# Kernel tuning notes

Measured on AMD Instinct MI355X. Metric: run time of the kernel, lower is better.

Reference implementation:

```python
import jax, jax.numpy as jnp
import numpy as np

TEMPERATURE = 2.0

def setup_inputs() -> dict:
    key = jax.random.key(0)
    x = jax.random.normal(key, (8192, 512), dtype=jnp.float32)
    return {"x": x}

def reference(x) -> jnp.ndarray:
    # torch.pdist(x, p=2).pow(2) == squared euclidean distance over pairs i<j
    n = x.shape[0]
    sq = jnp.sum(x * x, axis=1)                       # [N]
    d2 = sq[:, None] + sq[None, :] - 2.0 * (x @ x.T)  # [N, N]
    d2 = jnp.maximum(d2, 0.0)                         # numerical clamp
    mask = jnp.triu(jnp.ones((n, n), dtype=jnp.bool_), k=1)  # strict upper tri = pdist pairs
    num_pairs = n * (n - 1) // 2
    e = jnp.where(mask, jnp.exp(-TEMPERATURE * d2), 0.0)
    return jnp.log(jnp.sum(e) / num_pairs)
```

## Files before the change

### kernel.cpp

```cpp
#include <hip/hip_runtime.h>
#include <hip/hip_fp8.h>
#include <math.h>

#define N 8192
#define D 512
#define TT 64
#define NT 2080
#define NEG_INF_SENT (-3.0e38f)
#define SCALE1 0x7F7F7F7F

typedef __attribute__((ext_vector_type(8))) int int8x;
typedef __attribute__((ext_vector_type(16))) float f32x16;

#define AS1 __attribute__((address_space(1)))
#define AS3 __attribute__((address_space(3)))

__device__ inline void lse_merge(float& m1, float& s1, float m2, float s2) {
    float M = fmaxf(m1, m2);
    s1 = s1 * __expf(m1 - M) + s2 * __expf(m2 - M);
    m1 = M;
}

__global__ __launch_bounds__(256) void cast_rowsq_kernel(const float* __restrict__ x,
                                                         unsigned char* __restrict__ xb,
                                                         float* __restrict__ sq) {
#pragma unroll
    for (int g4 = 0; g4 < 4; ++g4) {
        int row = blockIdx.x * 16 + g4 * 4 + (threadIdx.x >> 6);
        int lane = threadIdx.x & 63;
        const float4* xr = (const float4*)(x + (size_t)row * D);
        float4 a = xr[lane * 2], b = xr[lane * 2 + 1];
        float v[8] = {a.x, a.y, a.z, a.w, b.x, b.y, b.z, b.w};
        float s = 0.f;
        unsigned int byt[8];
#pragma unroll
        for (int e = 0; e < 8; ++e) {
            s += v[e] * v[e];
            __hip_fp8_e4m3 f8(v[e]);
            byt[e] = (unsigned int)f8.__x;
        }
        uint2 pk;
        pk.x = byt[0] | (byt[1] << 8) | (byt[2] << 16) | (byt[3] << 24);
        pk.y = byt[4] | (byt[5] << 8) | (byt[6] << 16) | (byt[7] << 24);
        int g = row >> 5, rl = row & 31;
        int c = lane >> 3;
        int l5 = (lane >> 2) & 1;
        int h = (lane >> 1) & 1;
        int bb = (lane & 1) << 3;
        size_t addr = ((size_t)((g * 8 + c) * 2 + h) << 10) + ((l5 * 32 + rl) << 4) + bb;
        *(uint2*)(xb + addr) = pk;
#pragma unroll
        for (int off = 32; off > 0; off >>= 1) s += __shfl_down(s, off, 64);
        if (lane == 0) sq[row] = s;
    }
}

__global__ __launch_bounds__(256, 2) void pair_mfma_kernel(const unsigned char* __restrict__ xb,
                                                           const float* __restrict__ sq,
                                                           float* __restrict__ bm,
                                                           float* __restrict__ bs) {
    __shared__ __align__(16) unsigned char lds[2][32][1024];

    const int p = blockIdx.x;
    const int b = (p & 7) * 260 + (p >> 3);
    int bi = 0;
    while ((bi + 1) * (2 * TT - bi) / 2 <= b) ++bi;
    const int bj = bi + (b - bi * (2 * TT - bi + 1) / 2);
    const int i0 = bi * 128, j0 = bj * 128;
    const int gA = i0 >> 5, gB = j0 >> 5;

    const int tid = threadIdx.x;
    const int lane = tid & 63;
    const int w = tid >> 6;
    const int wy = w >> 1, wx = w & 1;
    const int l31 = lane & 31;
    const int l5 = lane >> 5;

    f32x16 acc[2][2];
#pragma unroll
    for (int mi = 0; mi < 2; ++mi)
#pragma unroll
        for (int ni = 0; ni < 2; ++ni)
#pragma unroll
            for (int r = 0; r < 16; ++r) acc[mi][ni][r] = 0.f;

    auto stage = [&](int C, int buf) {
#pragma unroll
        for (int u = 0; u < 8; ++u) {
            int f = (w << 3) | u;
            int side = f >> 4;
            int g = (f >> 2) & 3;
            int cc = (f >> 1) & 1;
            int h = f & 1;
            int grp = (side ? gB : gA) + g;
            int cg = C * 2 + cc;
            const unsigned char* src = xb + (((size_t)((grp * 8 + cg) * 2 + h)) << 10)
                                          + (lane << 4);
            __builtin_amdgcn_global_load_lds((const AS1 void*)src,
                                             (AS3 void*)&lds[buf][f][0], 16, 0, 0);
        }
    };

    stage(0, 0);
    __syncthreads();

    for (int C = 0; C < 4; ++C) {
        const int cur = C & 1;
        if (C < 3) stage(C + 1, cur ^ 1);
#pragma unroll
        for (int cc = 0; cc < 2; ++cc) {
            int8x af[2], bf[2];
#pragma unroll
            for (int mi = 0; mi < 2; ++mi) {
                int f = ((wy * 2 + mi) << 2) | (cc << 1);
                uint4 lo = *(const uint4*)&lds[cur][f][lane << 4];
                uint4 hi = *(const uint4*)&lds[cur][f + 1][lane << 4];
                af[mi][0] = lo.x; af[mi][1] = lo.y; af[mi][2] = lo.z; af[mi][3] = lo.w;
                af[mi][4] = hi.x; af[mi][5] = hi.y; af[mi][6] = hi.z; af[mi][7] = hi.w;
            }
#pragma unroll
            for (int ni = 0; ni < 2; ++ni) {
                int f = 16 | ((wx * 2 + ni) << 2) | (cc << 1);
                uint4 lo = *(const uint4*)&lds[cur][f][lane << 4];
                uint4 hi = *(const uint4*)&lds[cur][f + 1][lane << 4];
                bf[ni][0] = lo.x; bf[ni][1] = lo.y; bf[ni][2] = lo.z; bf[ni][3] = lo.w;
                bf[ni][4] = hi.x; bf[ni][5] = hi.y; bf[ni][6] = hi.z; bf[ni][7] = hi.w;
            }
#pragma unroll
            for (int mi = 0; mi < 2; ++mi)
#pragma unroll
                for (int ni = 0; ni < 2; ++ni)
                    acc[mi][ni] = __builtin_amdgcn_mfma_scale_f32_32x32x64_f8f6f4(
                        af[mi], bf[ni], acc[mi][ni], 0, 0, 0, SCALE1, 0, SCALE1);
        }
        __syncthreads();
    }

    const bool offdiag = (bi != bj);
    float sqj[2];
#pragma unroll
    for (int ni = 0; ni < 2; ++ni) sqj[ni] = sq[j0 + wx * 64 + ni * 32 + l31];

    float m = NEG_INF_SENT;
#pragma unroll
    for (int mi = 0; mi < 2; ++mi) {
#pragma unroll
        for (int r = 0; r < 16; ++r) {
            int row32 = (r & 3) + 8 * (r >> 2) + 4 * l5;
            int i = i0 + wy * 64 + mi * 32 + row32;
            float sqi = sq[i];
#pragma unroll
            for (int ni = 0; ni < 2; ++ni) {
                int j = j0 + wx * 64 + ni * 32 + l31;
                float d2 = fmaxf(sqi + sqj[ni] - 2.f * acc[mi][ni][r], 0.f);
                float tv = (offdiag || j > i) ? (-2.0f * d2) : NEG_INF_SENT;
                acc[mi][ni][r] = tv;
                m = fmaxf(m, tv);
            }
        }
    }
    float s = 0.f;
#pragma unroll
    for (int mi = 0; mi < 2; ++mi)
#pragma unroll
        for (int ni = 0; ni < 2; ++ni)
#pragma unroll
            for (int r = 0; r < 16; ++r)
                s += __expf(acc[mi][ni][r] - m);

#pragma unroll
    for (int off = 32; off > 0; off >>= 1) {
        float m2 = __shfl_down(m, off, 64);
        float s2 = __shfl_down(s, off, 64);
        lse_merge(m, s, m2, s2);
    }
    __shared__ float rm[4], rs[4];
    if (lane == 0) { rm[w] = m; rs[w] = s; }
    __syncthreads();
    if (tid == 0) {
#pragma unroll
        for (int v = 1; v < 4; ++v) lse_merge(rm[0], rs[0], rm[v], rs[v]);
        bm[p] = rm[0];
        bs[p] = rs[0];
    }
}

__global__ __launch_bounds__(256) void finalize_kernel(const float* __restrict__ bm,
                                                       const float* __restrict__ bs,
                                                       int nblocks,
                                                       float* __restrict__ out) {
    const int tid = threadIdx.x;
    float m = NEG_INF_SENT, s = 0.f;
    for (int b = tid; b < nblocks; b += 256) lse_merge(m, s, bm[b], bs[b]);
#pragma unroll
    for (int off = 32; off > 0; off >>= 1) {
        float m2 = __shfl_down(m, off, 64);
        float s2 = __shfl_down(s, off, 64);
        lse_merge(m, s, m2, s2);
    }
    __shared__ float rm[4], rs[4];
    if ((tid & 63) == 0) { rm[tid >> 6] = m; rs[tid >> 6] = s; }
    __syncthreads();
    if (tid == 0) {
#pragma unroll
        for (int v = 1; v < 4; ++v) lse_merge(rm[0], rs[0], rm[v], rs[v]);
        const float log_num_pairs = 17.3285362f;
        out[0] = rm[0] + logf(rs[0]) - log_num_pairs;
    }
}

extern "C" void kernel_launch(void* const* d_in, const int* in_sizes, int n_in,
                              void* d_out, int out_size, void* d_ws, size_t ws_size,
                              hipStream_t stream) {
    const float* x = (const float*)d_in[0];
    float* out = (float*)d_out;

    const size_t xb_bytes = (size_t)N * D;
    unsigned char* xb = (unsigned char*)d_ws;
    float* sq = (float*)((char*)d_ws + xb_bytes);
    float* bm = sq + N;
    float* bs = bm + NT;

    cast_rowsq_kernel<<<N / 16, 256, 0, stream>>>(x, xb, sq);
    pair_mfma_kernel<<<NT, 256, 0, stream>>>(xb, sq, bm, bs);
    finalize_kernel<<<1, 256, 0, stream>>>(bm, bs, NT, out);
}
```

Before: 103.9 us.

## Load MFMA operands directly from global into registers, dropping LDS staging

The pair kernel no longer stages fp8 tiles through double-buffered LDS with global_load_lds. Each wave now loads its A/B fragments straight from global memory into registers, prefetching the next K-chunk while issuing MFMAs on the current one. This removes the LDS traffic and the per-chunk block barriers, and the occupancy hint is raised to 3 blocks per SU. The cost is that waves sharing rows or columns re-read the same data from global/L2 instead of sharing it through LDS, and register pressure rises. The cast kernel's address formula is rewritten in an equivalent form.

```diff
diff --git a/kernel.cpp b/kernel.cpp
--- a/kernel.cpp
+++ b/kernel.cpp
@@ -11,9 +11,6 @@
 
 typedef __attribute__((ext_vector_type(8))) int int8x;
 typedef __attribute__((ext_vector_type(16))) float f32x16;
-
-#define AS1 __attribute__((address_space(1)))
-#define AS3 __attribute__((address_space(3)))
 
 __device__ inline void lse_merge(float& m1, float& s1, float m2, float s2) {
     float M = fmaxf(m1, m2);
@@ -47,7 +44,7 @@
         int l5 = (lane >> 2) & 1;
         int h = (lane >> 1) & 1;
         int bb = (lane & 1) << 3;
-        size_t addr = ((size_t)((g * 8 + c) * 2 + h) << 10) + ((l5 * 32 + rl) << 4) + bb;
+        size_t addr = ((size_t)(g * 16 + c * 2 + h) << 10) + ((l5 * 32 + rl) << 4) + bb;
         *(uint2*)(xb + addr) = pk;
 #pragma unroll
         for (int off = 32; off > 0; off >>= 1) s += __shfl_down(s, off, 64);
@@ -55,12 +52,10 @@
     }
 }
 
-__global__ __launch_bounds__(256, 2) void pair_mfma_kernel(const unsigned char* __restrict__ xb,
+__global__ __launch_bounds__(256, 3) void pair_mfma_kernel(const unsigned char* __restrict__ xb,
                                                            const float* __restrict__ sq,
                                                            float* __restrict__ bm,
                                                            float* __restrict__ bs) {
-    __shared__ __align__(16) unsigned char lds[2][32][1024];
-
     const int p = blockIdx.x;
     const int b = (p & 7) * 260 + (p >> 3);
     int bi = 0;
@@ -76,6 +71,15 @@
     const int l31 = lane & 31;
     const int l5 = lane >> 5;
 
+    int aOff[2][2], bOff[2][2];
+#pragma unroll
+    for (int mi = 0; mi < 2; ++mi)
+#pragma unroll
+        for (int h = 0; h < 2; ++h) {
+            aOff[mi][h] = (((gA + 2 * wy + mi) * 16 + h) << 10) + (lane << 4);
+            bOff[mi][h] = (((gB + 2 * wx + mi) * 16 + h) << 10) + (lane << 4);
+        }
+
     f32x16 acc[2][2];
 #pragma unroll
     for (int mi = 0; mi < 2; ++mi)
@@ -84,56 +88,34 @@
 #pragma unroll
             for (int r = 0; r < 16; ++r) acc[mi][ni][r] = 0.f;
 
-    auto stage = [&](int C, int buf) {
-#pragma unroll
-        for (int u = 0; u < 8; ++u) {
-            int f = (w << 3) | u;
-            int side = f >> 4;
-            int g = (f >> 2) & 3;
-            int cc = (f >> 1) & 1;
-            int h = f & 1;
-            int grp = (side ? gB : gA) + g;
-            int cg = C * 2 + cc;
-            const unsigned char* src = xb + (((size_t)((grp * 8 + cg) * 2 + h)) << 10)
-                                          + (lane << 4);
-            __builtin_amdgcn_global_load_lds((const AS1 void*)src,
-                                             (AS3 void*)&lds[buf][f][0], 16, 0, 0);
+    int8x af[2], bf[2];
+    auto load_chunk = [&](int c) {
+        const int co = c << 11;
+#pragma unroll
+        for (int mi = 0; mi < 2; ++mi) {
+            uint4 alo = *(const uint4*)(xb + aOff[mi][0] + co);
+            uint4 ahi = *(const uint4*)(xb + aOff[mi][1] + co);
+            uint4 blo = *(const uint4*)(xb + bOff[mi][0] + co);
+            uint4 bhi = *(const uint4*)(xb + bOff[mi][1] + co);
+            af[mi][0] = alo.x; af[mi][1] = alo.y; af[mi][2] = alo.z; af[mi][3] = alo.w;
+            af[mi][4] = ahi.x; af[mi][5] = ahi.y; af[mi][6] = ahi.z; af[mi][7] = ahi.w;
+            bf[mi][0] = blo.x; bf[mi][1] = blo.y; bf[mi][2] = blo.z; bf[mi][3] = blo.w;
+            bf[mi][4] = bhi.x; bf[mi][5] = bhi.y; bf[mi][6] = bhi.z; bf[mi][7] = bhi.w;
         }
     };
 
-    stage(0, 0);
-    __syncthreads();
-
-    for (int C = 0; C < 4; ++C) {
-        const int cur = C & 1;
-        if (C < 3) stage(C + 1, cur ^ 1);
-#pragma unroll
-        for (int cc = 0; cc < 2; ++cc) {
-            int8x af[2], bf[2];
-#pragma unroll
-            for (int mi = 0; mi < 2; ++mi) {
-                int f = ((wy * 2 + mi) << 2) | (cc << 1);
-                uint4 lo = *(const uint4*)&lds[cur][f][lane << 4];
-                uint4 hi = *(const uint4*)&lds[cur][f + 1][lane << 4];
-                af[mi][0] = lo.x; af[mi][1] = lo.y; af[mi][2] = lo.z; af[mi][3] = lo.w;
-                af[mi][4] = hi.x; af[mi][5] = hi.y; af[mi][6] = hi.z; af[mi][7] = hi.w;
-            }
-#pragma unroll
-            for (int ni = 0; ni < 2; ++ni) {
-                int f = 16 | ((wx * 2 + ni) << 2) | (cc << 1);
-                uint4 lo = *(const uint4*)&lds[cur][f][lane << 4];
-                uint4 hi = *(const uint4*)&lds[cur][f + 1][lane << 4];
-                bf[ni][0] = lo.x; bf[ni][1] = lo.y; bf[ni][2] = lo.z; bf[ni][3] = lo.w;
-                bf[ni][4] = hi.x; bf[ni][5] = hi.y; bf[ni][6] = hi.z; bf[ni][7] = hi.w;
-            }
-#pragma unroll
-            for (int mi = 0; mi < 2; ++mi)
-#pragma unroll
-                for (int ni = 0; ni < 2; ++ni)
-                    acc[mi][ni] = __builtin_amdgcn_mfma_scale_f32_32x32x64_f8f6f4(
-                        af[mi], bf[ni], acc[mi][ni], 0, 0, 0, SCALE1, 0, SCALE1);
-        }
-        __syncthreads();
+    load_chunk(0);
+#pragma unroll
+    for (int c = 0; c < 8; ++c) {
+        int8x ca[2], cb[2];
+        ca[0] = af[0]; ca[1] = af[1]; cb[0] = bf[0]; cb[1] = bf[1];
+        if (c < 7) load_chunk(c + 1);
+#pragma unroll
+        for (int mi = 0; mi < 2; ++mi)
+#pragma unroll
+            for (int ni = 0; ni < 2; ++ni)
+                acc[mi][ni] = __builtin_amdgcn_mfma_scale_f32_32x32x64_f8f6f4(
+                    ca[mi], cb[ni], acc[mi][ni], 0, 0, 0, SCALE1, 0, SCALE1);
     }
 
     const bool offdiag = (bi != bj);
```

Measured after the change: 111.1 us. +6.9%, slower.
